# Kernel optimization log

Measured on AMD Instinct MI355X. Metric: run time of the kernel, lower is better.

The kernel has to match this reference:

```python
import jax, jax.numpy as jnp
import numpy as np

INF = 1e38  # matches torch source constant


def setup_inputs() -> dict:
    key = jax.random.key(0)
    k1, k2, k3 = jax.random.split(key, 3)
    B, N, D = 16, 2048, 512
    query = jax.random.normal(k1, (B, N, D), dtype=jnp.float32)
    # nn.Linear(dims, dims, bias=False): weight [out, in] = [D, D]
    W_in = jax.random.normal(k2, (D, D), dtype=jnp.float32) * (1.0 / np.sqrt(D))
    # nn.Linear(2*dims, dims, bias=False): weight [D, 2D]
    W_out = jax.random.normal(k3, (D, 2 * D), dtype=jnp.float32) * (1.0 / np.sqrt(2 * D))
    return {"query": query, "W_in": W_in, "W_out": W_out}


def reference(query, W_in, W_out):
    B, N, D = query.shape
    # linear_in: y = x @ W^T
    q = jnp.einsum("bnd,ed->bne", query, W_in)  # [B, N, D]
    # full QK^T scores
    scores = jnp.einsum("bnd,bmd->bnm", q, q)  # [B, N, N]
    # torch: scores[:, triu_mask] = -INF  -> mask upper triangle INCLUDING diagonal
    mask = jnp.triu(jnp.ones((N, N), dtype=bool))
    scores = jnp.where(mask, -INF, scores)
    weights = jax.nn.softmax(scores, axis=-1)
    # row 0 is all -INF -> softmax gives uniform; torch zeroes it explicitly
    weights = weights.at[:, 0, :].set(0.0)
    mix = jnp.einsum("bnm,bmd->bnd", weights, q)  # [B, N, D]
    combined = jnp.concatenate([mix, q], axis=-1)  # [B, N, 2D]
    # linear_out (no activation since activation=None)
    output = jnp.einsum("bnc,dc->bnd", combined, W_out)  # [B, N, D]
    return output
```

## Files before the change

kernel.cpp:

```cpp
#include <hip/hip_runtime.h>

typedef _Float16 f16;
typedef _Float16 half8 __attribute__((ext_vector_type(8)));
typedef _Float16 half4 __attribute__((ext_vector_type(4)));
typedef float floatx4 __attribute__((ext_vector_type(4)));

#define MFMA16(a, b, c) __builtin_amdgcn_mfma_f32_16x16x32_f16(a, b, c, 0, 0, 0)

union H8 { half8 v; f16 e[8]; };

__device__ __forceinline__ void gload16(const void* g, void* l) {
    __builtin_amdgcn_global_load_lds((const __attribute__((address_space(1))) void*)g,
                                     (__attribute__((address_space(3))) void*)l, 16, 0, 0);
}

__global__ __launch_bounds__(256) void k_cvt(const float* __restrict__ query,
                                             const float* __restrict__ Wi,
                                             const float* __restrict__ Wo,
                                             f16* __restrict__ q16,
                                             f16* __restrict__ W16)
{
    int i = blockIdx.x * 256 + threadIdx.x;
    const float4* src;
    f16* dst;
    if (i < 4194304) { src = (const float4*)query + i; dst = q16 + (size_t)i * 4; }
    else if (i < 4259840) { int j = i - 4194304; src = (const float4*)Wi + j; dst = W16 + (size_t)j * 4; }
    else { int j = i - 4259840; src = (const float4*)Wo + j; dst = W16 + 262144 + (size_t)j * 4; }
    float4 v = *src;
    half4 h = {(f16)v.x, (f16)v.y, (f16)v.z, (f16)v.w};
    *reinterpret_cast<half4*>(dst) = h;
}

__global__ __launch_bounds__(256) void k_qin(const f16* __restrict__ q16,
                                             const f16* __restrict__ W16,
                                             f16* __restrict__ comb,
                                             f16* __restrict__ qT)
{
    __shared__ char sm[65536];
    const int tid = threadIdx.x, lane = tid & 63, w = tid >> 6;
    const int l15 = lane & 15, quad = lane >> 4;
    const int id = blockIdx.x, xcd = id & 7, u = id >> 3;
    const int mbase = (xcd * 32 + (u >> 2)) * 128;
    const int nbase = (u & 3) * 128;
    const int wm = (w & 1) * 64, wn = (w >> 1) * 64;
    const int ia = wm >> 4, jb = wn >> 4;

    floatx4 acc[4][4];
#pragma unroll
    for (int i = 0; i < 4; ++i)
#pragma unroll
        for (int j = 0; j < 4; ++j) acc[i][j] = (floatx4)0.f;

    auto STAGE = [&](int k0, int bsel) {
        f16* At = (f16*)(sm + bsel * 32768);
        f16* Bt = At + 8192;
#pragma unroll
        for (int jr = 0; jr < 4; ++jr) {
            int bi = jr * 4 + w, i2 = bi >> 1, s = bi & 1;
            gload16(q16 + (size_t)(mbase + i2 * 16 + l15) * 512 + k0 + s * 32 + quad * 8, At + bi * 512);
            gload16(W16 + (size_t)(nbase + i2 * 16 + l15) * 512 + k0 + s * 32 + quad * 8, Bt + bi * 512);
        }
    };

    STAGE(0, 0);
    __syncthreads();
    for (int it = 0; it < 8; ++it) {
        const int cur = it & 1;
        if (it < 7) STAGE((it + 1) * 64, cur ^ 1);
        f16* At = (f16*)(sm + cur * 32768);
        f16* Bt = At + 8192;
#pragma unroll
        for (int s = 0; s < 2; ++s) {
            half8 a[4], bf[4];
#pragma unroll
            for (int i = 0; i < 4; ++i)
                a[i] = *reinterpret_cast<half8*>(At + ((ia + i) * 2 + s) * 512 + lane * 8);
#pragma unroll
            for (int j = 0; j < 4; ++j)
                bf[j] = *reinterpret_cast<half8*>(Bt + ((jb + j) * 2 + s) * 512 + lane * 8);
#pragma unroll
            for (int i = 0; i < 4; ++i)
#pragma unroll
                for (int j = 0; j < 4; ++j)
                    acc[i][j] = MFMA16(a[i], bf[j], acc[i][j]);
        }
        __syncthreads();
    }
    const int bb = mbase >> 11, tb = mbase & 2047;
    f16* ct = (f16*)sm;
#pragma unroll
    for (int i = 0; i < 4; ++i)
#pragma unroll
        for (int j = 0; j < 4; ++j)
#pragma unroll
            for (int r = 0; r < 4; ++r)
                ct[(wm + i * 16 + quad * 4 + r) * 136 + wn + j * 16 + l15] = (f16)acc[i][j][r];
    __syncthreads();
#pragma unroll
    for (int it = 0; it < 8; ++it) {
        int c = it * 256 + tid, r = c >> 4, c8 = (c & 15) << 3;
        *reinterpret_cast<half8*>(comb + (size_t)(mbase + r) * 1024 + 512 + nbase + c8) =
            *reinterpret_cast<half8*>(ct + r * 136 + c8);
    }
    __syncthreads();
#pragma unroll
    for (int i = 0; i < 4; ++i)
#pragma unroll
        for (int j = 0; j < 4; ++j) {
            half4 h = {(f16)acc[i][j][0], (f16)acc[i][j][1], (f16)acc[i][j][2], (f16)acc[i][j][3]};
            *reinterpret_cast<half4*>(ct + (wn + j * 16 + l15) * 136 + wm + i * 16 + quad * 4) = h;
        }
    __syncthreads();
#pragma unroll
    for (int it = 0; it < 8; ++it) {
        int c = it * 256 + tid, dd = c >> 4, tc = (c & 15) << 3;
        *reinterpret_cast<half8*>(qT + ((size_t)bb * 512 + nbase + dd) * 2048 + tb + tc) =
            *reinterpret_cast<half8*>(ct + dd * 136 + tc);
    }
}

__global__ __launch_bounds__(256) void k_sgemm(const f16* __restrict__ comb,
                                               float* __restrict__ Sg, int batch0)
{
    __shared__ char sm[65536];
    const int tid = threadIdx.x, lane = tid & 63, w = tid >> 6;
    const int l15 = lane & 15, quad = lane >> 4;
    const int wm = (w & 1) * 64, wn = (w >> 1) * 64;
    const int ia = wm >> 4, jb = wn >> 4;

    int bx = blockIdx.y, mt = 0;
    while ((mt + 1) * (mt + 2) / 2 <= bx) ++mt;
    const int nt = bx - mt * (mt + 1) / 2;
    const int b = batch0 + blockIdx.x;
    const f16* qa = comb + ((size_t)b * 2048 + mt * 128) * 1024 + 512;
    const f16* qb = comb + ((size_t)b * 2048 + nt * 128) * 1024 + 512;

    floatx4 acc[4][4];
#pragma unroll
    for (int i = 0; i < 4; ++i)
#pragma unroll
        for (int j = 0; j < 4; ++j) acc[i][j] = (floatx4)0.f;

    auto STAGE = [&](int k0, int bsel) {
        f16* At = (f16*)(sm + bsel * 32768);
        f16* Bt = At + 8192;
#pragma unroll
        for (int jr = 0; jr < 4; ++jr) {
            int bi = jr * 4 + w, i2 = bi >> 1, s = bi & 1;
            gload16(qa + (size_t)(i2 * 16 + l15) * 1024 + k0 + s * 32 + quad * 8, At + bi * 512);
            gload16(qb + (size_t)(i2 * 16 + l15) * 1024 + k0 + s * 32 + quad * 8, Bt + bi * 512);
        }
    };

    STAGE(0, 0);
    __syncthreads();
    for (int it = 0; it < 8; ++it) {
        const int cur = it & 1;
        if (it < 7) STAGE((it + 1) * 64, cur ^ 1);
        f16* At = (f16*)(sm + cur * 32768);
        f16* Bt = At + 8192;
#pragma unroll
        for (int s = 0; s < 2; ++s) {
            half8 a[4], bf[4];
#pragma unroll
            for (int i = 0; i < 4; ++i)
                a[i] = *reinterpret_cast<half8*>(At + ((ia + i) * 2 + s) * 512 + lane * 8);
#pragma unroll
            for (int j = 0; j < 4; ++j)
                bf[j] = *reinterpret_cast<half8*>(Bt + ((jb + j) * 2 + s) * 512 + lane * 8);
#pragma unroll
            for (int i = 0; i < 4; ++i)
#pragma unroll
                for (int j = 0; j < 4; ++j)
                    acc[i][j] = MFMA16(a[i], bf[j], acc[i][j]);
        }
        __syncthreads();
    }
    float* St = Sg + ((size_t)blockIdx.x * 136 + bx) * 16384;
    float* cf = (float*)sm;
    for (int pass = 0; pass < 2; ++pass) {
        __syncthreads();
        if ((w & 1) == pass) {
#pragma unroll
            for (int i = 0; i < 4; ++i)
#pragma unroll
                for (int j = 0; j < 4; ++j)
#pragma unroll
                    for (int r = 0; r < 4; ++r)
                        cf[(i * 16 + quad * 4 + r) * 132 + wn + j * 16 + l15] = acc[i][j][r];
        }
        __syncthreads();
#pragma unroll
        for (int it = 0; it < 8; ++it) {
            int c = it * 256 + tid, row = c >> 5, c4 = (c & 31) << 2;
            __builtin_nontemporal_store(
                *reinterpret_cast<floatx4*>(cf + row * 132 + c4),
                reinterpret_cast<floatx4*>(St + (size_t)(pass * 64 + row) * 128 + c4));
        }
    }
}

__global__ __launch_bounds__(256) void k_softmax(float* Sg)
{
    const int tid = threadIdx.x, lane = tid & 63, w = tid >> 6;
    const int row = blockIdx.x * 4 + w;
    const int gb = blockIdx.y;
    const int mt = row >> 7;
    const size_t tbase = ((size_t)gb * 136 + (size_t)(mt * (mt + 1)) / 2) * 16384;
    const int padlen = (mt + 1) * 128;
    const int r128 = (row & 127) * 128;
    f16* Ph = (f16*)Sg;

    float sv[32];
    float m = -1e38f;
#pragma unroll
    for (int it = 0; it < 32; ++it) {
        int c = it * 64 + lane;
        float p = -1e38f;
        if (c < row) {
            p = Sg[tbase + (size_t)(c >> 7) * 16384 + r128 + (c & 127)];
            m = fmaxf(m, p);
        }
        sv[it] = p;
    }
#pragma unroll
    for (int msk = 32; msk >= 1; msk >>= 1) m = fmaxf(m, __shfl_xor(m, msk));
    float l = 0.f;
#pragma unroll
    for (int it = 0; it < 32; ++it) {
        int c = it * 64 + lane;
        float p = 0.f;
        if (c < row) { p = __expf(sv[it] - m); l += p; }
        sv[it] = p;
    }
#pragma unroll
    for (int msk = 32; msk >= 1; msk >>= 1) l += __shfl_xor(l, msk);
    const float invl = (row > 0) ? 1.f / l : 0.f;
#pragma unroll
    for (int it = 0; it < 32; ++it) {
        int c = it * 64 + lane;
        if (c < padlen)
            Ph[2 * (tbase + (size_t)(c >> 7) * 16384 + r128) + (c & 127)] = (f16)(sv[it] * invl);
    }
}

__global__ __launch_bounds__(256) void k_pv(const float* Sg,
                                            const f16* __restrict__ qT,
                                            f16* __restrict__ comb, int batch0)
{
    __shared__ char sm[65536];
    const int tid = threadIdx.x, lane = tid & 63, w = tid >> 6;
    const int l15 = lane & 15, quad = lane >> 4;
    const int wm = (w & 1) * 64, wn = (w >> 1) * 64;
    const int ia = wm >> 4, jb = wn >> 4;
    const int id = blockIdx.x;
    const int p = id & 7, nb = (id >> 3) & 3, gb = id >> 5;
    const int b = batch0 + gb;
    const f16* Ph = (const f16*)(Sg + (size_t)gb * 136 * 16384);
    const f16* qTb = qT + ((size_t)b * 512 + nb * 128) * 2048;

    for (int t = 0; t < 2; ++t) {
        const int mt = t ? (15 - p) : p;
        const int tb0 = mt * (mt + 1) / 2;
        const int kit = (mt + 1) * 2;

        floatx4 acc[4][4];
#pragma unroll
        for (int i = 0; i < 4; ++i)
#pragma unroll
            for (int j = 0; j < 4; ++j) acc[i][j] = (floatx4)0.f;

        auto STAGE = [&](int it, int bsel) {
            f16* At = (f16*)(sm + bsel * 32768);
            f16* Bt = At + 8192;
            const int k0 = it * 64;
            const int tt = tb0 + (k0 >> 7), c0 = k0 & 64;
#pragma unroll
            for (int jr = 0; jr < 4; ++jr) {
                int bi = jr * 4 + w, i2 = bi >> 1, s = bi & 1;
                gload16(Ph + 2 * ((size_t)tt * 16384 + (size_t)(i2 * 16 + l15) * 128) + c0 + s * 32 + quad * 8,
                        At + bi * 512);
                gload16(qTb + (size_t)(i2 * 16 + l15) * 2048 + k0 + s * 32 + quad * 8, Bt + bi * 512);
            }
        };

        STAGE(0, 0);
        __syncthreads();
        for (int it = 0; it < kit; ++it) {
            const int cur = it & 1;
            if (it + 1 < kit) STAGE(it + 1, cur ^ 1);
            f16* At = (f16*)(sm + cur * 32768);
            f16* Bt = At + 8192;
#pragma unroll
            for (int s = 0; s < 2; ++s) {
                half8 a[4], bf[4];
#pragma unroll
                for (int i = 0; i < 4; ++i)
                    a[i] = *reinterpret_cast<half8*>(At + ((ia + i) * 2 + s) * 512 + lane * 8);
#pragma unroll
                for (int j = 0; j < 4; ++j)
                    bf[j] = *reinterpret_cast<half8*>(Bt + ((jb + j) * 2 + s) * 512 + lane * 8);
#pragma unroll
                for (int i = 0; i < 4; ++i)
#pragma unroll
                    for (int j = 0; j < 4; ++j)
                        acc[i][j] = MFMA16(a[i], bf[j], acc[i][j]);
            }
            __syncthreads();
        }

        f16* ct = (f16*)sm;
#pragma unroll
        for (int i = 0; i < 4; ++i)
#pragma unroll
            for (int j = 0; j < 4; ++j)
#pragma unroll
                for (int r = 0; r < 4; ++r)
                    ct[(wm + i * 16 + quad * 4 + r) * 136 + wn + j * 16 + l15] = (f16)acc[i][j][r];
        __syncthreads();
#pragma unroll
        for (int it = 0; it < 8; ++it) {
            int c = it * 256 + tid, r = c >> 4, c8 = (c & 15) << 3;
            *reinterpret_cast<half8*>(comb + ((size_t)b * 2048 + mt * 128 + r) * 1024 + nb * 128 + c8) =
                *reinterpret_cast<half8*>(ct + r * 136 + c8);
        }
        __syncthreads();
    }
}

__global__ __launch_bounds__(256) void k_out(const f16* __restrict__ comb,
                                             const f16* __restrict__ Wo16,
                                             float* __restrict__ out)
{
    __shared__ char sm[65536];
    const int tid = threadIdx.x, lane = tid & 63, w = tid >> 6;
    const int l15 = lane & 15, quad = lane >> 4;
    const int id = blockIdx.x, xcd = id & 7, u = id >> 3;
    const int mbase = (xcd * 32 + (u >> 2)) * 128;
    const int nbase = (u & 3) * 128;
    const int wm = (w & 1) * 64, wn = (w >> 1) * 64;
    const int ia = wm >> 4, jb = wn >> 4;

    floatx4 acc[4][4];
#pragma unroll
    for (int i = 0; i < 4; ++i)
#pragma unroll
        for (int j = 0; j < 4; ++j) acc[i][j] = (floatx4)0.f;

    auto STAGE = [&](int k0, int bsel) {
        f16* At = (f16*)(sm + bsel * 32768);
        f16* Bt = At + 8192;
#pragma unroll
        for (int jr = 0; jr < 4; ++jr) {
            int bi = jr * 4 + w, i2 = bi >> 1, s = bi & 1;
            gload16(comb + (size_t)(mbase + i2 * 16 + l15) * 1024 + k0 + s * 32 + quad * 8,
                    At + bi * 512);
            gload16(Wo16 + (size_t)(nbase + i2 * 16 + l15) * 1024 + k0 + s * 32 + quad * 8,
                    Bt + bi * 512);
        }
    };

    STAGE(0, 0);
    __syncthreads();
    for (int it = 0; it < 16; ++it) {
        const int cur = it & 1;
        if (it < 15) STAGE((it + 1) * 64, cur ^ 1);
        f16* At = (f16*)(sm + cur * 32768);
        f16* Bt = At + 8192;
#pragma unroll
        for (int s = 0; s < 2; ++s) {
            half8 a[4], bf[4];
#pragma unroll
            for (int i = 0; i < 4; ++i)
                a[i] = *reinterpret_cast<half8*>(At + ((ia + i) * 2 + s) * 512 + lane * 8);
#pragma unroll
            for (int j = 0; j < 4; ++j)
                bf[j] = *reinterpret_cast<half8*>(Bt + ((jb + j) * 2 + s) * 512 + lane * 8);
#pragma unroll
            for (int i = 0; i < 4; ++i)
#pragma unroll
                for (int j = 0; j < 4; ++j)
                    acc[i][j] = MFMA16(a[i], bf[j], acc[i][j]);
        }
        __syncthreads();
    }
    float* cf = (float*)sm;
    for (int pass = 0; pass < 2; ++pass) {
        __syncthreads();
        if ((w & 1) == pass) {
#pragma unroll
            for (int i = 0; i < 4; ++i)
#pragma unroll
                for (int j = 0; j < 4; ++j)
#pragma unroll
                    for (int r = 0; r < 4; ++r)
                        cf[(i * 16 + quad * 4 + r) * 132 + wn + j * 16 + l15] = acc[i][j][r];
        }
        __syncthreads();
#pragma unroll
        for (int it = 0; it < 8; ++it) {
            int c = it * 256 + tid, row = c >> 5, c4 = (c & 31) << 2;
            __builtin_nontemporal_store(
                *reinterpret_cast<floatx4*>(cf + row * 132 + c4),
                reinterpret_cast<floatx4*>(out + (size_t)(mbase + pass * 64 + row) * 512 + nbase + c4));
        }
    }
}

extern "C" void kernel_launch(void* const* d_in, const int* in_sizes, int n_in,
                              void* d_out, int out_size, void* d_ws, size_t ws_size,
                              hipStream_t stream)
{
    const float* query = (const float*)d_in[0];
    const float* W_in  = (const float*)d_in[1];
    const float* W_out = (const float*)d_in[2];
    float* out = (float*)d_out;

    const size_t XOFF = 102236160ull;
    f16* comb = (f16*)d_ws;
    f16* qT   = comb + (size_t)32768 * 1024;
    f16* W16  = qT + (size_t)16 * 512 * 2048;
    f16* q16  = (f16*)((char*)d_ws + XOFF);
    const size_t sgb = 136ull * 16384 * 4;
    int ng;
    if (ws_size >= XOFF + 16 * sgb)      ng = 16;
    else if (ws_size >= XOFF + 8 * sgb)  ng = 8;
    else                                 ng = 4;
    float* Sg = (float*)((char*)d_ws + XOFF);

    k_cvt<<<17152, 256, 0, stream>>>(query, W_in, W_out, q16, W16);
    k_qin<<<1024, 256, 0, stream>>>(q16, W16, comb, qT);
    for (int g = 0; g < 16 / ng; ++g) {
        k_sgemm<<<dim3(ng, 136), 256, 0, stream>>>(comb, Sg, g * ng);
        k_softmax<<<dim3(512, ng), 256, 0, stream>>>(Sg);
        k_pv<<<32 * ng, 256, 0, stream>>>(Sg, qT, comb, g * ng);
    }
    k_out<<<1024, 256, 0, stream>>>(comb, W16 + 262144, out);
}
```

Before: 458.0 us.

## Fuse score GEMM with online softmax, deferring normalization to the PV kernel

Replaces the separate score GEMM, fp32 score buffer and softmax kernel with one kernel that computes each 64-row strip's causal score tiles, keeps running max and sum, and writes unnormalized fp16 exponentials plus per-tile rescale factors and final row sums. The PV kernel then rescales its accumulators at tile boundaries and divides by the row sum at the end. This removes the fp32 score write/read round trip and the per-batch-group launch loop. The cost is that each block walks its score tiles serially, with extra syncs per tile, and the grid is only 512 blocks whose work varies by strip.

```diff
diff --git a/kernel.cpp b/kernel.cpp
--- a/kernel.cpp
+++ b/kernel.cpp
@@ -6,8 +6,6 @@
 typedef float floatx4 __attribute__((ext_vector_type(4)));
 
 #define MFMA16(a, b, c) __builtin_amdgcn_mfma_f32_16x16x32_f16(a, b, c, 0, 0, 0)
-
-union H8 { half8 v; f16 e[8]; };
 
 __device__ __forceinline__ void gload16(const void* g, void* l) {
     __builtin_amdgcn_global_load_lds((const __attribute__((address_space(1))) void*)g,
@@ -119,134 +117,176 @@
     }
 }
 
-__global__ __launch_bounds__(256) void k_sgemm(const f16* __restrict__ comb,
-                                               float* __restrict__ Sg, int batch0)
-{
-    __shared__ char sm[65536];
+__global__ __launch_bounds__(256) void k_sgemmsm(const f16* __restrict__ comb,
+                                                 f16* __restrict__ Pd,
+                                                 float* __restrict__ Rt,
+                                                 float* __restrict__ Lt)
+{
+    __shared__ char sm[51200];
     const int tid = threadIdx.x, lane = tid & 63, w = tid >> 6;
     const int l15 = lane & 15, quad = lane >> 4;
-    const int wm = (w & 1) * 64, wn = (w >> 1) * 64;
-    const int ia = wm >> 4, jb = wn >> 4;
-
-    int bx = blockIdx.y, mt = 0;
-    while ((mt + 1) * (mt + 2) / 2 <= bx) ++mt;
-    const int nt = bx - mt * (mt + 1) / 2;
-    const int b = batch0 + blockIdx.x;
-    const f16* qa = comb + ((size_t)b * 2048 + mt * 128) * 1024 + 512;
-    const f16* qb = comb + ((size_t)b * 2048 + nt * 128) * 1024 + 512;
-
-    floatx4 acc[4][4];
+    const int id = blockIdx.x;
+    const int b = id & 15, s_ = id >> 4;
+    const int mt = 15 - (s_ >> 1), h = s_ & 1;
+    const int qrow0 = mt * 128 + h * 64;
+    const int tb0 = mt * (mt + 1) / 2;
+    const f16* qa = comb + ((size_t)b * 2048 + qrow0) * 1024 + 512;
+    float* redm = (float*)(sm + 49152);
+    float* reds = (float*)(sm + 50176);
+
+    float m_run[4][4], l_run[4][4];
 #pragma unroll
     for (int i = 0; i < 4; ++i)
 #pragma unroll
-        for (int j = 0; j < 4; ++j) acc[i][j] = (floatx4)0.f;
-
-    auto STAGE = [&](int k0, int bsel) {
-        f16* At = (f16*)(sm + bsel * 32768);
-        f16* Bt = At + 8192;
-#pragma unroll
-        for (int jr = 0; jr < 4; ++jr) {
-            int bi = jr * 4 + w, i2 = bi >> 1, s = bi & 1;
-            gload16(qa + (size_t)(i2 * 16 + l15) * 1024 + k0 + s * 32 + quad * 8, At + bi * 512);
-            gload16(qb + (size_t)(i2 * 16 + l15) * 1024 + k0 + s * 32 + quad * 8, Bt + bi * 512);
-        }
-    };
-
-    STAGE(0, 0);
-    __syncthreads();
-    for (int it = 0; it < 8; ++it) {
-        const int cur = it & 1;
-        if (it < 7) STAGE((it + 1) * 64, cur ^ 1);
-        f16* At = (f16*)(sm + cur * 32768);
-        f16* Bt = At + 8192;
-#pragma unroll
-        for (int s = 0; s < 2; ++s) {
-            half8 a[4], bf[4];
-#pragma unroll
-            for (int i = 0; i < 4; ++i)
-                a[i] = *reinterpret_cast<half8*>(At + ((ia + i) * 2 + s) * 512 + lane * 8);
-#pragma unroll
-            for (int j = 0; j < 4; ++j)
-                bf[j] = *reinterpret_cast<half8*>(Bt + ((jb + j) * 2 + s) * 512 + lane * 8);
-#pragma unroll
-            for (int i = 0; i < 4; ++i)
-#pragma unroll
-                for (int j = 0; j < 4; ++j)
-                    acc[i][j] = MFMA16(a[i], bf[j], acc[i][j]);
-        }
-        __syncthreads();
-    }
-    float* St = Sg + ((size_t)blockIdx.x * 136 + bx) * 16384;
-    float* cf = (float*)sm;
-    for (int pass = 0; pass < 2; ++pass) {
-        __syncthreads();
-        if ((w & 1) == pass) {
-#pragma unroll
-            for (int i = 0; i < 4; ++i)
-#pragma unroll
-                for (int j = 0; j < 4; ++j)
-#pragma unroll
-                    for (int r = 0; r < 4; ++r)
-                        cf[(i * 16 + quad * 4 + r) * 132 + wn + j * 16 + l15] = acc[i][j][r];
-        }
-        __syncthreads();
-#pragma unroll
+        for (int r = 0; r < 4; ++r) { m_run[i][r] = -1e38f; l_run[i][r] = 0.f; }
+
+    for (int nt = 0; nt <= mt; ++nt) {
+        const f16* qb = comb + ((size_t)b * 2048 + nt * 128) * 1024 + 512;
+        floatx4 acc[4][2];
+#pragma unroll
+        for (int i = 0; i < 4; ++i)
+#pragma unroll
+            for (int j = 0; j < 2; ++j) acc[i][j] = (floatx4)0.f;
+
+        auto STAGE = [&](int k0, int bsel) {
+            f16* At = (f16*)(sm + bsel * 24576);
+            f16* Bt = At + 4096;
+#pragma unroll
+            for (int jr = 0; jr < 2; ++jr) {
+                int ab = jr * 4 + w, i2 = ab >> 1, sa = ab & 1;
+                gload16(qa + (size_t)(i2 * 16 + l15) * 1024 + k0 + sa * 32 + quad * 8, At + ab * 512);
+            }
+#pragma unroll
+            for (int jr = 0; jr < 4; ++jr) {
+                int bi = jr * 4 + w, i2 = bi >> 1, sb = bi & 1;
+                gload16(qb + (size_t)(i2 * 16 + l15) * 1024 + k0 + sb * 32 + quad * 8, Bt + bi * 512);
+            }
+        };
+
+        STAGE(0, 0);
+        __syncthreads();
         for (int it = 0; it < 8; ++it) {
-            int c = it * 256 + tid, row = c >> 5, c4 = (c & 31) << 2;
-            __builtin_nontemporal_store(
-                *reinterpret_cast<floatx4*>(cf + row * 132 + c4),
-                reinterpret_cast<floatx4*>(St + (size_t)(pass * 64 + row) * 128 + c4));
-        }
-    }
-}
-
-__global__ __launch_bounds__(256) void k_softmax(float* Sg)
-{
-    const int tid = threadIdx.x, lane = tid & 63, w = tid >> 6;
-    const int row = blockIdx.x * 4 + w;
-    const int gb = blockIdx.y;
-    const int mt = row >> 7;
-    const size_t tbase = ((size_t)gb * 136 + (size_t)(mt * (mt + 1)) / 2) * 16384;
-    const int padlen = (mt + 1) * 128;
-    const int r128 = (row & 127) * 128;
-    f16* Ph = (f16*)Sg;
-
-    float sv[32];
-    float m = -1e38f;
-#pragma unroll
-    for (int it = 0; it < 32; ++it) {
-        int c = it * 64 + lane;
-        float p = -1e38f;
-        if (c < row) {
-            p = Sg[tbase + (size_t)(c >> 7) * 16384 + r128 + (c & 127)];
-            m = fmaxf(m, p);
-        }
-        sv[it] = p;
-    }
-#pragma unroll
-    for (int msk = 32; msk >= 1; msk >>= 1) m = fmaxf(m, __shfl_xor(m, msk));
-    float l = 0.f;
-#pragma unroll
-    for (int it = 0; it < 32; ++it) {
-        int c = it * 64 + lane;
-        float p = 0.f;
-        if (c < row) { p = __expf(sv[it] - m); l += p; }
-        sv[it] = p;
-    }
-#pragma unroll
-    for (int msk = 32; msk >= 1; msk >>= 1) l += __shfl_xor(l, msk);
-    const float invl = (row > 0) ? 1.f / l : 0.f;
-#pragma unroll
-    for (int it = 0; it < 32; ++it) {
-        int c = it * 64 + lane;
-        if (c < padlen)
-            Ph[2 * (tbase + (size_t)(c >> 7) * 16384 + r128) + (c & 127)] = (f16)(sv[it] * invl);
-    }
-}
-
-__global__ __launch_bounds__(256) void k_pv(const float* Sg,
+            const int cur = it & 1;
+            if (it < 7) STAGE((it + 1) * 64, cur ^ 1);
+            f16* At = (f16*)(sm + cur * 24576);
+            f16* Bt = At + 4096;
+#pragma unroll
+            for (int s = 0; s < 2; ++s) {
+                half8 a[4], bf[2];
+#pragma unroll
+                for (int i = 0; i < 4; ++i)
+                    a[i] = *reinterpret_cast<half8*>(At + (i * 2 + s) * 512 + lane * 8);
+#pragma unroll
+                for (int j = 0; j < 2; ++j)
+                    bf[j] = *reinterpret_cast<half8*>(Bt + ((w * 2 + j) * 2 + s) * 512 + lane * 8);
+#pragma unroll
+                for (int i = 0; i < 4; ++i)
+#pragma unroll
+                    for (int j = 0; j < 2; ++j)
+                        acc[i][j] = MFMA16(a[i], bf[j], acc[i][j]);
+            }
+            __syncthreads();
+        }
+
+        const bool diag = (nt == mt);
+        const int rb64 = h * 64;
+        float rfv[4][4], sum_p[4][4];
+        f16* ct = (f16*)sm;
+
+#pragma unroll
+        for (int i = 0; i < 4; ++i)
+#pragma unroll
+            for (int r = 0; r < 4; ++r) {
+                float v0 = acc[i][0][r], v1 = acc[i][1][r];
+                if (diag) {
+                    int rl = rb64 + i * 16 + quad * 4 + r;
+                    if (w * 32 + l15 >= rl)      v0 = -1e38f;
+                    if (w * 32 + 16 + l15 >= rl) v1 = -1e38f;
+                }
+                float mm = fmaxf(v0, v1);
+                mm = fmaxf(mm, __shfl_xor(mm, 1));
+                mm = fmaxf(mm, __shfl_xor(mm, 2));
+                mm = fmaxf(mm, __shfl_xor(mm, 4));
+                mm = fmaxf(mm, __shfl_xor(mm, 8));
+                sum_p[i][r] = mm;
+            }
+        if (l15 == 0)
+#pragma unroll
+            for (int i = 0; i < 4; ++i)
+#pragma unroll
+                for (int r = 0; r < 4; ++r)
+                    redm[w * 64 + i * 16 + quad * 4 + r] = sum_p[i][r];
+        __syncthreads();
+#pragma unroll
+        for (int i = 0; i < 4; ++i)
+#pragma unroll
+            for (int r = 0; r < 4; ++r) {
+                int row = i * 16 + quad * 4 + r;
+                float mm = fmaxf(fmaxf(redm[row], redm[64 + row]),
+                                 fmaxf(redm[128 + row], redm[192 + row]));
+                float mnew = fmaxf(m_run[i][r], mm);
+                float rf = __expf(m_run[i][r] - mnew);
+                m_run[i][r] = mnew;
+                rfv[i][r] = rf;
+                if (w == 0 && l15 == 0)
+                    Rt[((size_t)b * 16 + nt) * 2048 + qrow0 + row] = rf;
+            }
+#pragma unroll
+        for (int i = 0; i < 4; ++i)
+#pragma unroll
+            for (int r = 0; r < 4; ++r) {
+                int rl = rb64 + i * 16 + quad * 4 + r;
+                float ssum = 0.f;
+#pragma unroll
+                for (int j = 0; j < 2; ++j) {
+                    bool valid = !diag || (w * 32 + j * 16 + l15 < rl);
+                    float e = valid ? __expf(acc[i][j][r] - m_run[i][r]) : 0.f;
+                    ssum += e;
+                    ct[(i * 16 + quad * 4 + r) * 136 + w * 32 + j * 16 + l15] = (f16)e;
+                }
+                ssum += __shfl_xor(ssum, 1);
+                ssum += __shfl_xor(ssum, 2);
+                ssum += __shfl_xor(ssum, 4);
+                ssum += __shfl_xor(ssum, 8);
+                sum_p[i][r] = ssum;
+            }
+        if (l15 == 0)
+#pragma unroll
+            for (int i = 0; i < 4; ++i)
+#pragma unroll
+                for (int r = 0; r < 4; ++r)
+                    reds[w * 64 + i * 16 + quad * 4 + r] = sum_p[i][r];
+        __syncthreads();
+#pragma unroll
+        for (int i = 0; i < 4; ++i)
+#pragma unroll
+            for (int r = 0; r < 4; ++r) {
+                int row = i * 16 + quad * 4 + r;
+                float ts = (reds[row] + reds[64 + row]) + (reds[128 + row] + reds[192 + row]);
+                l_run[i][r] = l_run[i][r] * rfv[i][r] + ts;
+            }
+        f16* Pt = Pd + ((size_t)(b * 136 + tb0 + nt) << 14) + (size_t)rb64 * 128;
+#pragma unroll
+        for (int itp = 0; itp < 4; ++itp) {
+            int c = itp * 256 + tid, r_ = c >> 4, c8 = (c & 15) << 3;
+            *reinterpret_cast<half8*>(Pt + r_ * 128 + c8) =
+                *reinterpret_cast<half8*>(ct + r_ * 136 + c8);
+        }
+        __syncthreads();
+    }
+    if (w == 0 && l15 == 0)
+#pragma unroll
+        for (int i = 0; i < 4; ++i)
+#pragma unroll
+            for (int r = 0; r < 4; ++r)
+                Lt[(size_t)b * 2048 + qrow0 + i * 16 + quad * 4 + r] = l_run[i][r];
+}
+
+__global__ __launch_bounds__(256) void k_pv(const f16* __restrict__ Pd,
                                             const f16* __restrict__ qT,
-                                            f16* __restrict__ comb, int batch0)
+                                            f16* __restrict__ comb,
+                                            const float* __restrict__ Rt,
+                                            const float* __restrict__ Lt)
 {
     __shared__ char sm[65536];
     const int tid = threadIdx.x, lane = tid & 63, w = tid >> 6;
@@ -254,9 +294,8 @@
     const int wm = (w & 1) * 64, wn = (w >> 1) * 64;
     const int ia = wm >> 4, jb = wn >> 4;
     const int id = blockIdx.x;
-    const int p = id & 7, nb = (id >> 3) & 3, gb = id >> 5;
-    const int b = batch0 + gb;
-    const f16* Ph = (const f16*)(Sg + (size_t)gb * 136 * 16384);
+    const int p = id & 7, nb = (id >> 3) & 3, b = id >> 5;
+    const f16* Pdb = Pd + ((size_t)b * 136 << 14);
     const f16* qTb = qT + ((size_t)b * 512 + nb * 128) * 2048;
 
     for (int t = 0; t < 2; ++t) {
@@ -274,11 +313,11 @@
             f16* At = (f16*)(sm + bsel * 32768);
             f16* Bt = At + 8192;
             const int k0 = it * 64;
-            const int tt = tb0 + (k0 >> 7), c0 = k0 & 64;
 #pragma unroll
             for (int jr = 0; jr < 4; ++jr) {
                 int bi = jr * 4 + w, i2 = bi >> 1, s = bi & 1;
-                gload16(Ph + 2 * ((size_t)tt * 16384 + (size_t)(i2 * 16 + l15) * 128) + c0 + s * 32 + quad * 8,
+                gload16(Pdb + ((size_t)(tb0 + (k0 >> 7)) << 14) + (size_t)(i2 * 16 + l15) * 128
+                            + (k0 & 64) + s * 32 + quad * 8,
                         At + bi * 512);
                 gload16(qTb + (size_t)(i2 * 16 + l15) * 2048 + k0 + s * 32 + quad * 8, Bt + bi * 512);
             }
@@ -289,6 +328,17 @@
         for (int it = 0; it < kit; ++it) {
             const int cur = it & 1;
             if (it + 1 < kit) STAGE(it + 1, cur ^ 1);
+            if (it > 0 && (it & 1) == 0) {
+                const int tt = it >> 1;
+                const float* rbp = Rt + ((size_t)b * 16 + tt) * 2048 + mt * 128 + wm;
+#pragma unroll
+                for (int i = 0; i < 4; ++i) {
+                    floatx4 rv = *reinterpret_cast<const floatx4*>(rbp + i * 16 + quad * 4);
+#pragma unroll
+                    for (int j = 0; j < 4; ++j)
+                        acc[i][j] *= rv;
+                }
+            }
             f16* At = (f16*)(sm + cur * 32768);
             f16* Bt = At + 8192;
 #pragma unroll
@@ -310,13 +360,23 @@
         }
 
         f16* ct = (f16*)sm;
-#pragma unroll
-        for (int i = 0; i < 4; ++i)
+        const float* lbp = Lt + (size_t)b * 2048 + mt * 128 + wm;
+#pragma unroll
+        for (int i = 0; i < 4; ++i) {
+            floatx4 lv = *reinterpret_cast<const floatx4*>(lbp + i * 16 + quad * 4);
+            floatx4 inv;
+#pragma unroll
+            for (int r = 0; r < 4; ++r) {
+                int rowg = mt * 128 + wm + i * 16 + quad * 4 + r;
+                inv[r] = (rowg > 0) ? 1.f / lv[r] : 0.f;
+            }
 #pragma unroll
             for (int j = 0; j < 4; ++j)
 #pragma unroll
                 for (int r = 0; r < 4; ++r)
-                    ct[(wm + i * 16 + quad * 4 + r) * 136 + wn + j * 16 + l15] = (f16)acc[i][j][r];
+                    ct[(wm + i * 16 + quad * 4 + r) * 136 + wn + j * 16 + l15] =
+                        (f16)(acc[i][j][r] * inv[r]);
+        }
         __syncthreads();
 #pragma unroll
         for (int it = 0; it < 8; ++it) {
@@ -421,19 +481,13 @@
     f16* qT   = comb + (size_t)32768 * 1024;
     f16* W16  = qT + (size_t)16 * 512 * 2048;
     f16* q16  = (f16*)((char*)d_ws + XOFF);
-    const size_t sgb = 136ull * 16384 * 4;
-    int ng;
-    if (ws_size >= XOFF + 16 * sgb)      ng = 16;
-    else if (ws_size >= XOFF + 8 * sgb)  ng = 8;
-    else                                 ng = 4;
-    float* Sg = (float*)((char*)d_ws + XOFF);
+    f16* Pd   = (f16*)((char*)d_ws + XOFF);
+    float* Rt = (float*)((char*)d_ws + XOFF + 71303168ull);
+    float* Lt = (float*)((char*)d_ws + XOFF + 73400320ull);
 
     k_cvt<<<17152, 256, 0, stream>>>(query, W_in, W_out, q16, W16);
     k_qin<<<1024, 256, 0, stream>>>(q16, W16, comb, qT);
-    for (int g = 0; g < 16 / ng; ++g) {
-        k_sgemm<<<dim3(ng, 136), 256, 0, stream>>>(comb, Sg, g * ng);
-        k_softmax<<<dim3(512, ng), 256, 0, stream>>>(Sg);
-        k_pv<<<32 * ng, 256, 0, stream>>>(Sg, qT, comb, g * ng);
-    }
+    k_sgemmsm<<<512, 256, 0, stream>>>(comb, Pd, Rt, Lt);
+    k_pv<<<512, 256, 0, stream>>>(Pd, qT, comb, Rt, Lt);
     k_out<<<1024, 256, 0, stream>>>(comb, W16 + 262144, out);
 }
```

After: 541.8 us. 18.3% more time.

## Fuse tile-local softmax into score GEMM and rescale per tile in PV

Applied to the files above, without the earlier changes.

The QK^T GEMM now computes a causal-masked local softmax inside each 128x128 tile, keeping per-tile row max and sum and storing unnormalized fp16 exponentials instead of fp32 scores. A small stats kernel combines the per-tile maxima and sums into a per-tile scale factor. The PV GEMM applies that factor as each key tile's partial product finishes, adding it into a second accumulator. This removes the fp32 score round trip and the separate full-row softmax pass, and the workspace is no longer split into batch groups. In exchange PV holds twice as many accumulator registers, and fp16 exponentials relative to a tile-local max can lose precision.

```diff
diff --git a/kernel.cpp b/kernel.cpp
--- a/kernel.cpp
+++ b/kernel.cpp
@@ -4,10 +4,9 @@
 typedef _Float16 half8 __attribute__((ext_vector_type(8)));
 typedef _Float16 half4 __attribute__((ext_vector_type(4)));
 typedef float floatx4 __attribute__((ext_vector_type(4)));
+typedef unsigned int uintx4 __attribute__((ext_vector_type(4)));
 
 #define MFMA16(a, b, c) __builtin_amdgcn_mfma_f32_16x16x32_f16(a, b, c, 0, 0, 0)
-
-union H8 { half8 v; f16 e[8]; };
 
 __device__ __forceinline__ void gload16(const void* g, void* l) {
     __builtin_amdgcn_global_load_lds((const __attribute__((address_space(1))) void*)g,
@@ -119,8 +118,10 @@
     }
 }
 
-__global__ __launch_bounds__(256) void k_sgemm(const f16* __restrict__ comb,
-                                               float* __restrict__ Sg, int batch0)
+__global__ __launch_bounds__(256) void k_sgemmsm(const f16* __restrict__ comb,
+                                                 f16* __restrict__ Pd,
+                                                 float* __restrict__ Mt,
+                                                 float* __restrict__ Lt)
 {
     __shared__ char sm[65536];
     const int tid = threadIdx.x, lane = tid & 63, w = tid >> 6;
@@ -131,7 +132,7 @@
     int bx = blockIdx.y, mt = 0;
     while ((mt + 1) * (mt + 2) / 2 <= bx) ++mt;
     const int nt = bx - mt * (mt + 1) / 2;
-    const int b = batch0 + blockIdx.x;
+    const int b = blockIdx.x;
     const f16* qa = comb + ((size_t)b * 2048 + mt * 128) * 1024 + 512;
     const f16* qb = comb + ((size_t)b * 2048 + nt * 128) * 1024 + 512;
 
@@ -176,77 +177,111 @@
         }
         __syncthreads();
     }
-    float* St = Sg + ((size_t)blockIdx.x * 136 + bx) * 16384;
-    float* cf = (float*)sm;
-    for (int pass = 0; pass < 2; ++pass) {
-        __syncthreads();
-        if ((w & 1) == pass) {
-#pragma unroll
-            for (int i = 0; i < 4; ++i)
-#pragma unroll
-                for (int j = 0; j < 4; ++j)
-#pragma unroll
-                    for (int r = 0; r < 4; ++r)
-                        cf[(i * 16 + quad * 4 + r) * 132 + wn + j * 16 + l15] = acc[i][j][r];
-        }
-        __syncthreads();
-#pragma unroll
-        for (int it = 0; it < 8; ++it) {
-            int c = it * 256 + tid, row = c >> 5, c4 = (c & 31) << 2;
-            __builtin_nontemporal_store(
-                *reinterpret_cast<floatx4*>(cf + row * 132 + c4),
-                reinterpret_cast<floatx4*>(St + (size_t)(pass * 64 + row) * 128 + c4));
-        }
-    }
-}
-
-__global__ __launch_bounds__(256) void k_softmax(float* Sg)
-{
-    const int tid = threadIdx.x, lane = tid & 63, w = tid >> 6;
-    const int row = blockIdx.x * 4 + w;
-    const int gb = blockIdx.y;
-    const int mt = row >> 7;
-    const size_t tbase = ((size_t)gb * 136 + (size_t)(mt * (mt + 1)) / 2) * 16384;
-    const int padlen = (mt + 1) * 128;
-    const int r128 = (row & 127) * 128;
-    f16* Ph = (f16*)Sg;
-
-    float sv[32];
-    float m = -1e38f;
-#pragma unroll
-    for (int it = 0; it < 32; ++it) {
-        int c = it * 64 + lane;
-        float p = -1e38f;
-        if (c < row) {
-            p = Sg[tbase + (size_t)(c >> 7) * 16384 + r128 + (c & 127)];
-            m = fmaxf(m, p);
-        }
-        sv[it] = p;
-    }
-#pragma unroll
-    for (int msk = 32; msk >= 1; msk >>= 1) m = fmaxf(m, __shfl_xor(m, msk));
+
+    const bool diag = (nt == mt);
+    f16* ct = (f16*)sm;
+    float* redm = (float*)(sm + 40960);
+    float* reds = (float*)(sm + 43008);
+    const int hb = w & 1;
+
+    float wmax[4][4];
+#pragma unroll
+    for (int i = 0; i < 4; ++i)
+#pragma unroll
+        for (int r = 0; r < 4; ++r) {
+            const int rowl = wm + i * 16 + quad * 4 + r;
+            float mm = -1e38f;
+#pragma unroll
+            for (int j = 0; j < 4; ++j) {
+                float v = acc[i][j][r];
+                if (diag && (wn + j * 16 + l15) >= rowl) v = -1e38f;
+                mm = fmaxf(mm, v);
+            }
+            mm = fmaxf(mm, __shfl_xor(mm, 1));
+            mm = fmaxf(mm, __shfl_xor(mm, 2));
+            mm = fmaxf(mm, __shfl_xor(mm, 4));
+            mm = fmaxf(mm, __shfl_xor(mm, 8));
+            wmax[i][r] = mm;
+        }
+    if (l15 == 0)
+#pragma unroll
+        for (int i = 0; i < 4; ++i)
+#pragma unroll
+            for (int r = 0; r < 4; ++r)
+                redm[w * 64 + i * 16 + quad * 4 + r] = wmax[i][r];
+    __syncthreads();
+
+#pragma unroll
+    for (int i = 0; i < 4; ++i)
+#pragma unroll
+        for (int r = 0; r < 4; ++r) {
+            const int idx = i * 16 + quad * 4 + r;
+            const int rowl = wm + idx;
+            const float m = fmaxf(redm[hb * 64 + idx], redm[(hb + 2) * 64 + idx]);
+            float ssum = 0.f;
+#pragma unroll
+            for (int j = 0; j < 4; ++j) {
+                const int col = wn + j * 16 + l15;
+                const bool valid = !diag || (col < rowl);
+                float e = valid ? __expf(acc[i][j][r] - m) : 0.f;
+                ssum += e;
+                ct[rowl * 136 + col] = (f16)e;
+            }
+            ssum += __shfl_xor(ssum, 1);
+            ssum += __shfl_xor(ssum, 2);
+            ssum += __shfl_xor(ssum, 4);
+            ssum += __shfl_xor(ssum, 8);
+            wmax[i][r] = ssum;
+        }
+    if (l15 == 0)
+#pragma unroll
+        for (int i = 0; i < 4; ++i)
+#pragma unroll
+            for (int r = 0; r < 4; ++r)
+                reds[w * 64 + i * 16 + quad * 4 + r] = wmax[i][r];
+    __syncthreads();
+
+    if (tid < 128) {
+        const int h2 = tid >> 6, i2 = tid & 63;
+        const float mm = fmaxf(redm[h2 * 64 + i2], redm[(h2 + 2) * 64 + i2]);
+        const float ll = reds[h2 * 64 + i2] + reds[(h2 + 2) * 64 + i2];
+        const size_t o = (((size_t)b * 16 + nt) << 11) + mt * 128 + tid;
+        Mt[o] = mm;
+        Lt[o] = ll;
+    }
+    f16* Pt = Pd + ((size_t)(b * 136 + bx) << 14);
+#pragma unroll
+    for (int itp = 0; itp < 8; ++itp) {
+        int c = itp * 256 + tid, r_ = c >> 4, c8 = (c & 15) << 3;
+        __builtin_nontemporal_store(
+            *reinterpret_cast<uintx4*>(ct + r_ * 136 + c8),
+            reinterpret_cast<uintx4*>(Pt + r_ * 128 + c8));
+    }
+}
+
+__global__ __launch_bounds__(256) void k_stats(float* Mt, const float* __restrict__ Lt)
+{
+    const int b = blockIdx.x, row = blockIdx.y * 256 + threadIdx.x;
+    const int mtr = row >> 7;
+    float mv[16], lv[16];
+    for (int t = 0; t <= mtr; ++t) {
+        const size_t o = (((size_t)b * 16 + t) << 11) + row;
+        mv[t] = Mt[o];
+        lv[t] = Lt[o];
+    }
+    float M = -1e38f;
+    for (int t = 0; t <= mtr; ++t) M = fmaxf(M, mv[t]);
     float l = 0.f;
-#pragma unroll
-    for (int it = 0; it < 32; ++it) {
-        int c = it * 64 + lane;
-        float p = 0.f;
-        if (c < row) { p = __expf(sv[it] - m); l += p; }
-        sv[it] = p;
-    }
-#pragma unroll
-    for (int msk = 32; msk >= 1; msk >>= 1) l += __shfl_xor(l, msk);
-    const float invl = (row > 0) ? 1.f / l : 0.f;
-#pragma unroll
-    for (int it = 0; it < 32; ++it) {
-        int c = it * 64 + lane;
-        if (c < padlen)
-            Ph[2 * (tbase + (size_t)(c >> 7) * 16384 + r128) + (c & 127)] = (f16)(sv[it] * invl);
-    }
-}
-
-__global__ __launch_bounds__(256) void k_pv(const float* Sg,
+    for (int t = 0; t <= mtr; ++t) l += lv[t] * __expf(mv[t] - M);
+    const float invl = (l > 0.f) ? 1.f / l : 0.f;
+    for (int t = 0; t <= mtr; ++t)
+        Mt[(((size_t)b * 16 + t) << 11) + row] = __expf(mv[t] - M) * invl;
+}
+
+__global__ __launch_bounds__(256) void k_pv(const f16* __restrict__ Pd,
                                             const f16* __restrict__ qT,
-                                            f16* __restrict__ comb, int batch0)
+                                            f16* __restrict__ comb,
+                                            const float* __restrict__ Ft)
 {
     __shared__ char sm[65536];
     const int tid = threadIdx.x, lane = tid & 63, w = tid >> 6;
@@ -254,9 +289,8 @@
     const int wm = (w & 1) * 64, wn = (w >> 1) * 64;
     const int ia = wm >> 4, jb = wn >> 4;
     const int id = blockIdx.x;
-    const int p = id & 7, nb = (id >> 3) & 3, gb = id >> 5;
-    const int b = batch0 + gb;
-    const f16* Ph = (const f16*)(Sg + (size_t)gb * 136 * 16384);
+    const int p = id & 7, nb = (id >> 3) & 3, b = id >> 5;
+    const f16* Pdb = Pd + ((size_t)b * 136 << 14);
     const f16* qTb = qT + ((size_t)b * 512 + nb * 128) * 2048;
 
     for (int t = 0; t < 2; ++t) {
@@ -264,21 +298,21 @@
         const int tb0 = mt * (mt + 1) / 2;
         const int kit = (mt + 1) * 2;
 
-        floatx4 acc[4][4];
+        floatx4 acc[4][4], accT[4][4];
 #pragma unroll
         for (int i = 0; i < 4; ++i)
 #pragma unroll
-            for (int j = 0; j < 4; ++j) acc[i][j] = (floatx4)0.f;
+            for (int j = 0; j < 4; ++j) { acc[i][j] = (floatx4)0.f; accT[i][j] = (floatx4)0.f; }
 
         auto STAGE = [&](int it, int bsel) {
             f16* At = (f16*)(sm + bsel * 32768);
             f16* Bt = At + 8192;
             const int k0 = it * 64;
-            const int tt = tb0 + (k0 >> 7), c0 = k0 & 64;
 #pragma unroll
             for (int jr = 0; jr < 4; ++jr) {
                 int bi = jr * 4 + w, i2 = bi >> 1, s = bi & 1;
-                gload16(Ph + 2 * ((size_t)tt * 16384 + (size_t)(i2 * 16 + l15) * 128) + c0 + s * 32 + quad * 8,
+                gload16(Pdb + ((size_t)(tb0 + (k0 >> 7)) << 14) + (size_t)(i2 * 16 + l15) * 128
+                            + (k0 & 64) + s * 32 + quad * 8,
                         At + bi * 512);
                 gload16(qTb + (size_t)(i2 * 16 + l15) * 2048 + k0 + s * 32 + quad * 8, Bt + bi * 512);
             }
@@ -306,6 +340,19 @@
                     for (int j = 0; j < 4; ++j)
                         acc[i][j] = MFMA16(a[i], bf[j], acc[i][j]);
             }
+            if (it & 1) {
+                const int tt = it >> 1;
+                const float* fp = Ft + (((size_t)b * 16 + tt) << 11) + mt * 128 + wm;
+#pragma unroll
+                for (int i = 0; i < 4; ++i) {
+                    floatx4 fv = *reinterpret_cast<const floatx4*>(fp + i * 16 + quad * 4);
+#pragma unroll
+                    for (int j = 0; j < 4; ++j) {
+                        accT[i][j] += acc[i][j] * fv;
+                        acc[i][j] = (floatx4)0.f;
+                    }
+                }
+            }
             __syncthreads();
         }
 
@@ -316,7 +363,7 @@
             for (int j = 0; j < 4; ++j)
 #pragma unroll
                 for (int r = 0; r < 4; ++r)
-                    ct[(wm + i * 16 + quad * 4 + r) * 136 + wn + j * 16 + l15] = (f16)acc[i][j][r];
+                    ct[(wm + i * 16 + quad * 4 + r) * 136 + wn + j * 16 + l15] = (f16)accT[i][j][r];
         __syncthreads();
 #pragma unroll
         for (int it = 0; it < 8; ++it) {
@@ -421,19 +468,14 @@
     f16* qT   = comb + (size_t)32768 * 1024;
     f16* W16  = qT + (size_t)16 * 512 * 2048;
     f16* q16  = (f16*)((char*)d_ws + XOFF);
-    const size_t sgb = 136ull * 16384 * 4;
-    int ng;
-    if (ws_size >= XOFF + 16 * sgb)      ng = 16;
-    else if (ws_size >= XOFF + 8 * sgb)  ng = 8;
-    else                                 ng = 4;
-    float* Sg = (float*)((char*)d_ws + XOFF);
+    f16* Pd   = (f16*)((char*)d_ws + XOFF);
+    float* Mt = (float*)((char*)d_ws + XOFF + 71303168ull);
+    float* Lt = (float*)((char*)d_ws + XOFF + 73400320ull);
 
     k_cvt<<<17152, 256, 0, stream>>>(query, W_in, W_out, q16, W16);
     k_qin<<<1024, 256, 0, stream>>>(q16, W16, comb, qT);
-    for (int g = 0; g < 16 / ng; ++g) {
-        k_sgemm<<<dim3(ng, 136), 256, 0, stream>>>(comb, Sg, g * ng);
-        k_softmax<<<dim3(512, ng), 256, 0, stream>>>(Sg);
-        k_pv<<<32 * ng, 256, 0, stream>>>(Sg, qT, comb, g * ng);
-    }
+    k_sgemmsm<<<dim3(16, 136), 256, 0, stream>>>(comb, Pd, Mt, Lt);
+    k_stats<<<dim3(16, 8), 256, 0, stream>>>(Mt, Lt);
+    k_pv<<<512, 256, 0, stream>>>(Pd, qT, comb, Mt);
     k_out<<<1024, 256, 0, stream>>>(comb, W16 + 262144, out);
 }
```

Result: no change. 453.6 us (-1.0%).
